# Kernel optimization log

Hardware: AMD Instinct MI355X
Metric: run time of the kernel (lower is better)

The kernel has to match this reference:

```python
import jax, jax.numpy as jnp
import numpy as np

E = 1280   # embed_dim
H = 16     # num_heads
D = E // H # head_dim = 80
S = 3072   # total tokens


def _rotate_half(x):
    x1, x2 = x[..., : D // 2], x[..., D // 2:]
    return jnp.concatenate((-x2, x1), axis=-1)


def setup_inputs() -> dict:
    key = jax.random.key(0)
    ks = jax.random.split(key, 7)
    x = jax.random.normal(ks[0], (S, E), dtype=jnp.float32)
    # rotary embeddings: cos/sin of random angles, shape (S, head_dim)
    ang = jax.random.uniform(ks[1], (S, D), dtype=jnp.float32) * (2 * np.pi)
    cos = jnp.cos(ang)
    sin = jnp.sin(ang)
    # 8 variable-length segments covering all S tokens
    cu_seqlens = jnp.array([0, 256, 640, 1024, 1536, 1920, 2304, 2688, 3072], dtype=jnp.int32)
    qkv_w = jax.random.normal(ks[2], (3 * E, E), dtype=jnp.float32) * 0.02
    qkv_b = jax.random.normal(ks[3], (3 * E,), dtype=jnp.float32) * 0.02
    proj_w = jax.random.normal(ks[4], (E, E), dtype=jnp.float32) * 0.02
    proj_b = jax.random.normal(ks[5], (E,), dtype=jnp.float32) * 0.02
    return {"x": x, "cu_seqlens": cu_seqlens, "cos": cos, "sin": sin,
            "qkv_w": qkv_w, "qkv_b": qkv_b, "proj_w": proj_w, "proj_b": proj_b}


def reference(x, cu_seqlens, cos, sin, qkv_w, qkv_b, proj_w, proj_b):
    # QKV projection: (S, 3E)
    qkv = x @ qkv_w.T + qkv_b
    q, k, v = jnp.split(qkv, 3, axis=-1)
    q = q.reshape(S, H, D)
    k = k.reshape(S, H, D)
    v = v.reshape(S, H, D)
    # inline RoPE, broadcast over heads (cos/sin: (S,1,D))
    c = cos[:, None, :]
    s = sin[:, None, :]
    q = q * c + _rotate_half(q) * s
    k = k * c + _rotate_half(k) * s
    # block-diagonal varlen attention: tokens attend only within their segment
    seg_ids = jnp.searchsorted(cu_seqlens, jnp.arange(S), side="right")  # (S,)
    mask = seg_ids[:, None] == seg_ids[None, :]                           # (S,S)
    scale = 1.0 / jnp.sqrt(jnp.asarray(D, dtype=q.dtype))
    scores = jnp.einsum("qhd,khd->hqk", q, k) * scale                    # (H,S,S)
    neg = jnp.finfo(scores.dtype).min
    scores = jnp.where(mask[None, :, :], scores, neg)
    attn = jax.nn.softmax(scores, axis=-1)
    out = jnp.einsum("hqk,khd->qhd", attn, v).reshape(S, E)
    return out @ proj_w.T + proj_b
```

## Files before the change

kernel.cpp:

```cpp
#include <hip/hip_runtime.h>
#include <hip/hip_bf16.h>

#define S_LEN 3072
#define E_DIM 1280
#define NH 16
#define HD 80
#define HDP 96
#define QKV_N 3840

typedef unsigned short u16;
typedef unsigned int u32;
typedef __bf16 bf16x8 __attribute__((ext_vector_type(8)));
typedef float f32x4 __attribute__((ext_vector_type(4)));

__device__ __forceinline__ u16 bf16_bits(float f) {
  __hip_bfloat16 b = __float2bfloat16(f);
  return *reinterpret_cast<u16*>(&b);
}
__device__ __forceinline__ float bf16_to_f(u16 u) {
  unsigned int x = ((unsigned int)u) << 16;
  return __uint_as_float(x);
}
__device__ __forceinline__ void gload_lds16(const u16* g, u16* l) {
  __builtin_amdgcn_global_load_lds(
      (const __attribute__((address_space(1))) void*)g,
      (__attribute__((address_space(3))) void*)l, 16, 0, 0);
}
__device__ __forceinline__ int imin(int a, int b) { return a < b ? a : b; }

#define XB_F4    983040
#define WQKV_F4  1228800
#define WPROJ_F4 409600
__global__ __launch_bounds__(256) void f32_to_bf16_3(const float* __restrict__ sx,
                                                     const float* __restrict__ sq,
                                                     const float* __restrict__ sp,
                                                     u16* __restrict__ dst) {
  int i = blockIdx.x * 256 + threadIdx.x;
  float4 v;
  if (i < XB_F4) v = reinterpret_cast<const float4*>(sx)[i];
  else if (i < XB_F4 + WQKV_F4) v = reinterpret_cast<const float4*>(sq)[i - XB_F4];
  else v = reinterpret_cast<const float4*>(sp)[i - XB_F4 - WQKV_F4];
  ushort4 o;
  o.x = bf16_bits(v.x); o.y = bf16_bits(v.y); o.z = bf16_bits(v.z); o.w = bf16_bits(v.w);
  reinterpret_cast<ushort4*>(dst)[i] = o;
}

template<int OUT_F32>
__global__ __launch_bounds__(256) void gemm_nt(const u16* __restrict__ A,
                                               const u16* __restrict__ B,
                                               const float* __restrict__ bias,
                                               void* __restrict__ Cout,
                                               int M, int N, int K, int nbx) {
  __shared__ u16 As[128 * 64];
  __shared__ u16 Bs[128 * 64];
  const int t = threadIdx.x;
  const int lane = t & 63;
  const int wave = t >> 6;
  const int l15 = lane & 15, l4 = lane >> 4;
  const int wm = (wave >> 1) * 64, wn = (wave & 1) * 64;

  const int nwg = gridDim.x;
  const int lg = (blockIdx.x & 7) * (nwg >> 3) + (blockIdx.x >> 3);
  const int m0 = (lg / nbx) * 128, n0 = (lg % nbx) * 128;

  const u16* gA[4];
  const u16* gB[4];
  u16* lA[4];
  u16* lB[4];
  #pragma unroll
  for (int i = 0; i < 4; ++i) {
    const int c = i * 256 + t;
    const int row = c >> 3;
    const int col = ((c & 7) ^ (row & 7)) * 8;
    gA[i] = A + (size_t)(m0 + row) * K + col;
    gB[i] = B + (size_t)(n0 + row) * K + col;
    lA[i] = &As[c * 8];
    lB[i] = &Bs[c * 8];
  }

  int aoff[4][2], boff[4][2];
  #pragma unroll
  for (int i = 0; i < 4; ++i)
    #pragma unroll
    for (int kk = 0; kk < 2; ++kk) {
      aoff[i][kk] = (wm + i * 16 + l15) * 64 + ((kk * 4 + l4) ^ (l15 & 7)) * 8;
      boff[i][kk] = (wn + i * 16 + l15) * 64 + ((kk * 4 + l4) ^ (l15 & 7)) * 8;
    }

  f32x4 acc[4][4] = {};

  const int nk = K >> 6;
  for (int kt = 0; kt < nk; ++kt) {
    const int k0 = kt << 6;
    #pragma unroll
    for (int i = 0; i < 4; ++i) gload_lds16(gA[i] + k0, lA[i]);
    #pragma unroll
    for (int i = 0; i < 4; ++i) gload_lds16(gB[i] + k0, lB[i]);
    __syncthreads();
    bf16x8 af[4][2], bfr[4][2];
    #pragma unroll
    for (int i = 0; i < 4; ++i)
      #pragma unroll
      for (int kk = 0; kk < 2; ++kk) {
        af[i][kk]  = *reinterpret_cast<const bf16x8*>(&As[aoff[i][kk]]);
        bfr[i][kk] = *reinterpret_cast<const bf16x8*>(&Bs[boff[i][kk]]);
      }
    __builtin_amdgcn_s_setprio(1);
    #pragma unroll
    for (int kk = 0; kk < 2; ++kk)
      #pragma unroll
      for (int i = 0; i < 4; ++i)
        #pragma unroll
        for (int j = 0; j < 4; ++j)
          acc[i][j] = __builtin_amdgcn_mfma_f32_16x16x32_bf16(af[i][kk], bfr[j][kk],
                                                              acc[i][j], 0, 0, 0);
    __builtin_amdgcn_s_setprio(0);
    __syncthreads();
  }

  #pragma unroll
  for (int i = 0; i < 4; ++i) {
    #pragma unroll
    for (int j = 0; j < 4; ++j) {
      const int col = n0 + wn + j * 16 + l15;
      const float bv = bias[col];
      const int rowb = m0 + wm + i * 16 + l4 * 4;
      #pragma unroll
      for (int r = 0; r < 4; ++r) {
        float v = acc[i][j][r] + bv;
        if (OUT_F32)
          reinterpret_cast<float*>(Cout)[(size_t)(rowb + r) * N + col] = v;
        else
          reinterpret_cast<u16*>(Cout)[(size_t)(rowb + r) * N + col] = bf16_bits(v);
      }
    }
  }
}

#define ROPE_NB 12288
#define VT_NB   1920
__global__ __launch_bounds__(256) void rope_vt(const u16* __restrict__ qkv,
                                               const float* __restrict__ cosb,
                                               const float* __restrict__ sinb,
                                               u16* __restrict__ qp,
                                               u16* __restrict__ kp,
                                               u16* __restrict__ vt) {
  const int b = blockIdx.x;
  const int t = threadIdx.x;
  if (b < ROPE_NB) {
    const int h = b / 768;
    const int sl = t >> 6;
    const int p = t & 63;
    const int s = (b % 768) * 4 + sl;
    const size_t ib = (size_t)s * QKV_N + h * HD;
    const size_t ob = ((size_t)h * S_LEN + s) * HDP;
    if (p < 40) {
      const float scale = 0.1118033988749895f;
      float q1 = bf16_to_f(qkv[ib + p]);
      float q2 = bf16_to_f(qkv[ib + 40 + p]);
      float k1 = bf16_to_f(qkv[ib + E_DIM + p]);
      float k2 = bf16_to_f(qkv[ib + E_DIM + 40 + p]);
      float c1 = cosb[(size_t)s * HD + p],      s1 = sinb[(size_t)s * HD + p];
      float c2 = cosb[(size_t)s * HD + 40 + p], s2 = sinb[(size_t)s * HD + 40 + p];
      qp[ob + p]      = bf16_bits((q1 * c1 - q2 * s1) * scale);
      qp[ob + 40 + p] = bf16_bits((q2 * c2 + q1 * s2) * scale);
      kp[ob + p]      = bf16_bits(k1 * c1 - k2 * s1);
      kp[ob + 40 + p] = bf16_bits(k2 * c2 + k1 * s2);
    } else if (p < 48) {
      const int pd = HD + (p - 40) * 2;
      qp[ob + pd] = 0; qp[ob + pd + 1] = 0;
      kp[ob + pd] = 0; kp[ob + pd + 1] = 0;
    }
  } else {
    const int idx = (b - ROPE_NB) * 256 + t;
    const int d = idx % HD;
    const int h = (idx / HD) % NH;
    const int sb = idx / (HD * NH);
    const int s0 = sb * 8;
    if (s0 >= S_LEN) return;
    u16 bb[8];
    #pragma unroll
    for (int j = 0; j < 8; ++j)
      bb[j] = qkv[(size_t)(s0 + j) * QKV_N + 2 * E_DIM + h * HD + d];
    uint4 pk;
    pk.x = bb[0] | ((unsigned)bb[1] << 16);
    pk.y = bb[2] | ((unsigned)bb[3] << 16);
    pk.z = bb[4] | ((unsigned)bb[5] << 16);
    pk.w = bb[6] | ((unsigned)bb[7] << 16);
    *reinterpret_cast<uint4*>(&vt[((size_t)h * HD + d) * S_LEN + s0]) = pk;
  }
}

__global__ __launch_bounds__(256, 3) void attn_fwd(const u16* __restrict__ qp,
                                                   const u16* __restrict__ kp,
                                                   const u16* __restrict__ vt,
                                                   const int* __restrict__ cu, int ncu,
                                                   u16* __restrict__ ao) {
  __shared__ u16 Ks[64 * 128];
  __shared__ u16 Vs[80 * 64];
  __shared__ u16 Pl[4][16][72];

  const int lg = ((blockIdx.x & 7) * 96) + (blockIdx.x >> 3);
  const int h = lg / 48;
  const int q0 = (lg % 48) * 64;

  const int t = threadIdx.x;
  const int wave = t >> 6;
  const int lane = t & 63;
  const int l15 = lane & 15, l4 = lane >> 4;
  const int qr = q0 + wave * 16;

  int lo = 0, hi = S_LEN;
  for (int i = 0; i + 1 < ncu; ++i) {
    int a = cu[i], b = cu[i + 1];
    if (q0 >= a && q0 < b) { lo = a; hi = b; }
  }
  const int nt = (hi - lo + 63) >> 6;

  const u16* qh = qp + (size_t)h * S_LEN * HDP;
  const u16* kh = kp + (size_t)h * S_LEN * HDP;
  const u16* vh = vt + (size_t)h * HD * S_LEN;

  bf16x8 qf[3];
  #pragma unroll
  for (int c = 0; c < 3; ++c)
    qf[c] = *reinterpret_cast<const bf16x8*>(&qh[(size_t)(qr + l15) * HDP + c * 32 + l4 * 8]);

  int kr[3], kcc[3], kw[3];
  #pragma unroll
  for (int i = 0; i < 3; ++i) {
    const int c2 = i * 256 + t;
    kr[i] = c2 / 12; kcc[i] = c2 % 12;
    kw[i] = kr[i] * 128 + ((kcc[i] ^ (kr[i] & 7)) * 8);
  }
  int vd[3], vcc[3], vwo[3];
  #pragma unroll
  for (int i = 0; i < 3; ++i) {
    const int c2 = i * 256 + t;
    vd[i] = c2 >> 3; vcc[i] = c2 & 7;
    vwo[i] = vd[i] * 64 + ((vcc[i] ^ (vd[i] & 7)) * 8);
  }
  const bool v2 = (t < 128);

  {
    const int kbv = imin(lo, S_LEN - 64);
    bf16x8 kstg[3], vstg[3];
    #pragma unroll
    for (int i = 0; i < 3; ++i)
      kstg[i] = *reinterpret_cast<const bf16x8*>(
          &kh[(size_t)imin(lo + kr[i], S_LEN - 1) * HDP + kcc[i] * 8]);
    #pragma unroll
    for (int i = 0; i < 2; ++i)
      vstg[i] = *reinterpret_cast<const bf16x8*>(&vh[(size_t)vd[i] * S_LEN + kbv + vcc[i] * 8]);
    if (v2)
      vstg[2] = *reinterpret_cast<const bf16x8*>(&vh[(size_t)vd[2] * S_LEN + kbv + vcc[2] * 8]);
    #pragma unroll
    for (int i = 0; i < 3; ++i) *reinterpret_cast<bf16x8*>(&Ks[kw[i]]) = kstg[i];
    #pragma unroll
    for (int i = 0; i < 2; ++i) *reinterpret_cast<bf16x8*>(&Vs[vwo[i]]) = vstg[i];
    if (v2) *reinterpret_cast<bf16x8*>(&Vs[vwo[2]]) = vstg[2];
    __syncthreads();
  }

  f32x4 oacc[5] = {};
  float mrow = -INFINITY, lrow = 0.f;
  const float L2E = 1.4426950408889634f;

  int pwr[4];
  #pragma unroll
  for (int f = 0; f < 4; ++f)
    pwr[f] = ((f * 2 + (l4 >> 1)) ^ (l15 & 7)) * 8 + (l4 & 1) * 4;
  int prd[2];
  #pragma unroll
  for (int kc = 0; kc < 2; ++kc)
    prd[kc] = ((kc * 4 + l4) ^ (l15 & 7)) * 8;

  for (int ti = 0; ti < nt; ++ti) {
    const int kb = lo + ti * 64;
    const bool more = (ti + 1) < nt;

    bf16x8 kstg[3], vstg[3];
    if (more) {
      const int kb2 = kb + 64;
      const int kbv = imin(kb2, S_LEN - 64);
      #pragma unroll
      for (int i = 0; i < 3; ++i)
        kstg[i] = *reinterpret_cast<const bf16x8*>(
            &kh[(size_t)imin(kb2 + kr[i], S_LEN - 1) * HDP + kcc[i] * 8]);
      #pragma unroll
      for (int i = 0; i < 2; ++i)
        vstg[i] = *reinterpret_cast<const bf16x8*>(&vh[(size_t)vd[i] * S_LEN + kbv + vcc[i] * 8]);
      if (v2)
        vstg[2] = *reinterpret_cast<const bf16x8*>(&vh[(size_t)vd[2] * S_LEN + kbv + vcc[2] * 8]);
    }

    f32x4 sc[4];
    #pragma unroll
    for (int f = 0; f < 4; ++f) { f32x4 z = {0.f, 0.f, 0.f, 0.f}; sc[f] = z; }
    __builtin_amdgcn_s_setprio(1);
    #pragma unroll
    for (int f = 0; f < 4; ++f)
      #pragma unroll
      for (int c = 0; c < 3; ++c) {
        bf16x8 kf = *reinterpret_cast<const bf16x8*>(
            &Ks[(f * 16 + l15) * 128 + (((c * 4 + l4) ^ (l15 & 7)) * 8)]);
        sc[f] = __builtin_amdgcn_mfma_f32_16x16x32_bf16(kf, qf[c], sc[f], 0, 0, 0);
      }
    __builtin_amdgcn_s_setprio(0);

    if (kb + 64 > hi) {
      #pragma unroll
      for (int f = 0; f < 4; ++f)
        #pragma unroll
        for (int r = 0; r < 4; ++r)
          if (kb + f * 16 + l4 * 4 + r >= hi) sc[f][r] = -INFINITY;
    }

    float tm = -INFINITY;
    #pragma unroll
    for (int f = 0; f < 4; ++f)
      #pragma unroll
      for (int r = 0; r < 4; ++r) tm = fmaxf(tm, sc[f][r]);
    tm = fmaxf(tm, __shfl_xor(tm, 16, 64));
    tm = fmaxf(tm, __shfl_xor(tm, 32, 64));

    if (__any(tm > mrow + 8.f)) {
      float mn = fmaxf(mrow, tm);
      float corr = exp2f((mrow - mn) * L2E);
      mrow = mn;
      lrow *= corr;
      #pragma unroll
      for (int df = 0; df < 5; ++df)
        #pragma unroll
        for (int r = 0; r < 4; ++r) oacc[df][r] *= corr;
    }

    float rs = 0.f;
    #pragma unroll
    for (int f = 0; f < 4; ++f) {
      float p0 = exp2f((sc[f][0] - mrow) * L2E);
      float p1 = exp2f((sc[f][1] - mrow) * L2E);
      float p2 = exp2f((sc[f][2] - mrow) * L2E);
      float p3 = exp2f((sc[f][3] - mrow) * L2E);
      rs += (p0 + p1) + (p2 + p3);
      uint2 w;
      w.x = (u32)bf16_bits(p0) | ((u32)bf16_bits(p1) << 16);
      w.y = (u32)bf16_bits(p2) | ((u32)bf16_bits(p3) << 16);
      *reinterpret_cast<uint2*>(&Pl[wave][l15][pwr[f]]) = w;
    }
    rs += __shfl_xor(rs, 16, 64);
    rs += __shfl_xor(rs, 32, 64);
    lrow += rs;

    asm volatile("s_waitcnt lgkmcnt(0)" ::: "memory");

    __builtin_amdgcn_s_setprio(1);
    #pragma unroll
    for (int kc = 0; kc < 2; ++kc) {
      bf16x8 pf = *reinterpret_cast<const bf16x8*>(&Pl[wave][l15][prd[kc]]);
      #pragma unroll
      for (int df = 0; df < 5; ++df) {
        bf16x8 vf = *reinterpret_cast<const bf16x8*>(
            &Vs[(df * 16 + l15) * 64 + (((kc * 4 + l4) ^ (l15 & 7)) * 8)]);
        oacc[df] = __builtin_amdgcn_mfma_f32_16x16x32_bf16(vf, pf, oacc[df], 0, 0, 0);
      }
    }
    __builtin_amdgcn_s_setprio(0);

    if (more) {
      __syncthreads();
      #pragma unroll
      for (int i = 0; i < 3; ++i) *reinterpret_cast<bf16x8*>(&Ks[kw[i]]) = kstg[i];
      #pragma unroll
      for (int i = 0; i < 2; ++i) *reinterpret_cast<bf16x8*>(&Vs[vwo[i]]) = vstg[i];
      if (v2) *reinterpret_cast<bf16x8*>(&Vs[vwo[2]]) = vstg[2];
      __syncthreads();
    }
  }

  const float inv = 1.0f / lrow;
  #pragma unroll
  for (int df = 0; df < 5; ++df) {
    ushort4 o;
    o.x = bf16_bits(oacc[df][0] * inv);
    o.y = bf16_bits(oacc[df][1] * inv);
    o.z = bf16_bits(oacc[df][2] * inv);
    o.w = bf16_bits(oacc[df][3] * inv);
    *reinterpret_cast<ushort4*>(
        &ao[(size_t)(qr + l15) * E_DIM + h * HD + df * 16 + l4 * 4]) = o;
  }
}

extern "C" void kernel_launch(void* const* d_in, const int* in_sizes, int n_in,
                              void* d_out, int out_size, void* d_ws, size_t ws_size,
                              hipStream_t stream) {
  const float* x      = (const float*)d_in[0];
  const int*   cu     = (const int*)d_in[1];
  const float* cosb   = (const float*)d_in[2];
  const float* sinb   = (const float*)d_in[3];
  const float* qkv_w  = (const float*)d_in[4];
  const float* qkv_b  = (const float*)d_in[5];
  const float* proj_w = (const float*)d_in[6];
  const float* proj_b = (const float*)d_in[7];
  float* out = (float*)d_out;

  u16* xb     = (u16*)d_ws;
  u16* wqkvb  = xb     + (size_t)S_LEN * E_DIM;
  u16* wprojb = wqkvb  + (size_t)3 * E_DIM * E_DIM;
  u16* qkv    = wprojb + (size_t)E_DIM * E_DIM;
  u16* qp     = qkv    + (size_t)S_LEN * QKV_N;
  u16* kp     = qp     + (size_t)NH * S_LEN * HDP;
  u16* vt     = kp     + (size_t)NH * S_LEN * HDP;
  u16* attn   = vt     + (size_t)NH * HD * S_LEN;

  const int nf4 = XB_F4 + WQKV_F4 + WPROJ_F4;
  f32_to_bf16_3<<<nf4 / 256, 256, 0, stream>>>(x, qkv_w, proj_w, xb);

  gemm_nt<0><<<(QKV_N / 128) * (S_LEN / 128), 256, 0, stream>>>(
      xb, wqkvb, qkv_b, qkv, S_LEN, QKV_N, E_DIM, QKV_N / 128);

  rope_vt<<<ROPE_NB + VT_NB, 256, 0, stream>>>(qkv, cosb, sinb, qp, kp, vt);

  attn_fwd<<<NH * (S_LEN / 64), 256, 0, stream>>>(qp, kp, vt, cu, in_sizes[1], attn);

  gemm_nt<1><<<(E_DIM / 128) * (S_LEN / 128), 256, 0, stream>>>(
      attn, wprojb, proj_b, out, S_LEN, E_DIM, E_DIM, E_DIM / 128);
}
```

Before: 109.8 us.

## Fuse RoPE and V transpose into QKV GEMM epilogue via interleaved weight rows

Permutes the Q/K rows of the QKV weight and bias during the conversion pass so that rotate-half partner columns land in adjacent lanes. The QKV GEMM epilogue then applies RoPE with a lane shuffle and writes padded Q/K and transposed V directly. This removes the intermediate bf16 QKV buffer and the separate rope_vt kernel along with their global memory round trip. In exchange the epilogue issues scattered 2-byte stores and per-element cos/sin loads, and zeroing of the pad columns moves into the prep kernel.

After: 121.7 us. 10.9% more time.

```diff
diff --git a/kernel.cpp b/kernel.cpp
--- a/kernel.cpp
+++ b/kernel.cpp
@@ -28,28 +28,175 @@
 }
 __device__ __forceinline__ int imin(int a, int b) { return a < b ? a : b; }
 
+__device__ __forceinline__ int qk_orig(int c) {
+  if (c >= 2 * E_DIM) return c;
+  int h = c / 80, c80 = c % 80;
+  int p = c80 >> 1;
+  return h * 80 + ((c80 & 1) ? 40 + p : p);
+}
+
 #define XB_F4    983040
 #define WQKV_F4  1228800
 #define WPROJ_F4 409600
-__global__ __launch_bounds__(256) void f32_to_bf16_3(const float* __restrict__ sx,
-                                                     const float* __restrict__ sq,
-                                                     const float* __restrict__ sp,
-                                                     u16* __restrict__ dst) {
-  int i = blockIdx.x * 256 + threadIdx.x;
-  float4 v;
-  if (i < XB_F4) v = reinterpret_cast<const float4*>(sx)[i];
-  else if (i < XB_F4 + WQKV_F4) v = reinterpret_cast<const float4*>(sq)[i - XB_F4];
-  else v = reinterpret_cast<const float4*>(sp)[i - XB_F4 - WQKV_F4];
-  ushort4 o;
-  o.x = bf16_bits(v.x); o.y = bf16_bits(v.y); o.z = bf16_bits(v.z); o.w = bf16_bits(v.w);
-  reinterpret_cast<ushort4*>(dst)[i] = o;
-}
-
-template<int OUT_F32>
+#define CV_BLKS  10240
+#define PB_BLKS  15
+#define PAD_BLKS 768
+__global__ __launch_bounds__(256) void prep(const float* __restrict__ sx,
+                                            const float* __restrict__ sq,
+                                            const float* __restrict__ sp,
+                                            const float* __restrict__ qb,
+                                            u16* __restrict__ dst,
+                                            float* __restrict__ pb,
+                                            u16* __restrict__ qp,
+                                            u16* __restrict__ kp) {
+  const int b = blockIdx.x, t = threadIdx.x;
+  if (b < CV_BLKS) {
+    int i = b * 256 + t;
+    float4 v;
+    if (i < XB_F4) v = reinterpret_cast<const float4*>(sx)[i];
+    else if (i < XB_F4 + WQKV_F4) {
+      int j = i - XB_F4;
+      int row = j / 320, c4 = j % 320;
+      v = reinterpret_cast<const float4*>(sq)[(size_t)qk_orig(row) * 320 + c4];
+    } else v = reinterpret_cast<const float4*>(sp)[i - XB_F4 - WQKV_F4];
+    ushort4 o;
+    o.x = bf16_bits(v.x); o.y = bf16_bits(v.y); o.z = bf16_bits(v.z); o.w = bf16_bits(v.w);
+    reinterpret_cast<ushort4*>(dst)[i] = o;
+  } else if (b < CV_BLKS + PB_BLKS) {
+    int i = (b - CV_BLKS) * 256 + t;
+    if (i < QKV_N) pb[i] = qb[qk_orig(i)];
+  } else {
+    int u = (b - CV_BLKS - PB_BLKS) * 256 + t;
+    const int per = NH * S_LEN * 2;
+    u16* d = (u < per) ? qp : kp;
+    int r2 = (u < per) ? u : u - per;
+    int hs = r2 >> 1, half = r2 & 1;
+    uint4 z = {0u, 0u, 0u, 0u};
+    *reinterpret_cast<uint4*>(&d[(size_t)hs * HDP + 80 + half * 8]) = z;
+  }
+}
+
+__global__ __launch_bounds__(256) void gemm_qkv(const u16* __restrict__ A,
+                                                const u16* __restrict__ B,
+                                                const float* __restrict__ pb,
+                                                const float* __restrict__ cosb,
+                                                const float* __restrict__ sinb,
+                                                u16* __restrict__ qp,
+                                                u16* __restrict__ kp,
+                                                u16* __restrict__ vt) {
+  __shared__ u16 As[128 * 64];
+  __shared__ u16 Bs[128 * 64];
+  const int K = E_DIM;
+  const int t = threadIdx.x;
+  const int lane = t & 63;
+  const int wave = t >> 6;
+  const int l15 = lane & 15, l4 = lane >> 4;
+  const int wm = (wave >> 1) * 64, wn = (wave & 1) * 64;
+
+  const int nwg = gridDim.x;
+  const int lg = (blockIdx.x & 7) * (nwg >> 3) + (blockIdx.x >> 3);
+  const int m0 = (lg / 30) * 128, n0 = (lg % 30) * 128;
+
+  const u16* gA[4];
+  const u16* gB[4];
+  u16* lA[4];
+  u16* lB[4];
+  #pragma unroll
+  for (int i = 0; i < 4; ++i) {
+    const int c = i * 256 + t;
+    const int row = c >> 3;
+    const int col = ((c & 7) ^ (row & 7)) * 8;
+    gA[i] = A + (size_t)(m0 + row) * K + col;
+    gB[i] = B + (size_t)(n0 + row) * K + col;
+    lA[i] = &As[c * 8];
+    lB[i] = &Bs[c * 8];
+  }
+
+  int aoff[4][2], boff[4][2];
+  #pragma unroll
+  for (int i = 0; i < 4; ++i)
+    #pragma unroll
+    for (int kk = 0; kk < 2; ++kk) {
+      aoff[i][kk] = (wm + i * 16 + l15) * 64 + ((kk * 4 + l4) ^ (l15 & 7)) * 8;
+      boff[i][kk] = (wn + i * 16 + l15) * 64 + ((kk * 4 + l4) ^ (l15 & 7)) * 8;
+    }
+
+  f32x4 acc[4][4] = {};
+
+  const int nk = K >> 6;
+  for (int kt = 0; kt < nk; ++kt) {
+    const int k0 = kt << 6;
+    #pragma unroll
+    for (int i = 0; i < 4; ++i) gload_lds16(gA[i] + k0, lA[i]);
+    #pragma unroll
+    for (int i = 0; i < 4; ++i) gload_lds16(gB[i] + k0, lB[i]);
+    __syncthreads();
+    bf16x8 af[4][2], bfr[4][2];
+    #pragma unroll
+    for (int i = 0; i < 4; ++i)
+      #pragma unroll
+      for (int kk = 0; kk < 2; ++kk) {
+        af[i][kk]  = *reinterpret_cast<const bf16x8*>(&As[aoff[i][kk]]);
+        bfr[i][kk] = *reinterpret_cast<const bf16x8*>(&Bs[boff[i][kk]]);
+      }
+    __builtin_amdgcn_s_setprio(1);
+    #pragma unroll
+    for (int kk = 0; kk < 2; ++kk)
+      #pragma unroll
+      for (int i = 0; i < 4; ++i)
+        #pragma unroll
+        for (int j = 0; j < 4; ++j)
+          acc[i][j] = __builtin_amdgcn_mfma_f32_16x16x32_bf16(af[i][kk], bfr[j][kk],
+                                                              acc[i][j], 0, 0, 0);
+    __builtin_amdgcn_s_setprio(0);
+    __syncthreads();
+  }
+
+  const bool isqk = (n0 < 2 * E_DIM);
+  const bool isq  = (n0 < E_DIM);
+  const float scaleq = 0.1118033988749895f;
+  #pragma unroll
+  for (int i = 0; i < 4; ++i) {
+    const int srow = m0 + wm + i * 16 + l4 * 4;
+    #pragma unroll
+    for (int j = 0; j < 4; ++j) {
+      const int col = n0 + wn + j * 16 + l15;
+      const float bv = pb[col];
+      float vv[4];
+      #pragma unroll
+      for (int r = 0; r < 4; ++r) vv[r] = acc[i][j][r] + bv;
+      if (isqk) {
+        const int c80 = col % 80;
+        const int hh = col / 80;
+        const int parity = c80 & 1;
+        const int peff = (c80 >> 1) + (parity ? 40 : 0);
+        u16* dst = isq ? qp : kp;
+        const int hb = isq ? hh : hh - NH;
+        const float sc = isq ? scaleq : 1.0f;
+        #pragma unroll
+        for (int r = 0; r < 4; ++r) {
+          float pv = __shfl_xor(vv[r], 1, 64);
+          float cs = cosb[(size_t)(srow + r) * HD + peff];
+          float sn = sinb[(size_t)(srow + r) * HD + peff];
+          float o = parity ? fmaf(pv, sn, vv[r] * cs) : fmaf(-pv, sn, vv[r] * cs);
+          dst[((size_t)hb * S_LEN + srow + r) * HDP + c80] = bf16_bits(o * sc);
+        }
+      } else {
+        const int cv = col - 2 * E_DIM;
+        const int hb = cv / 80, d = cv % 80;
+        ushort4 o;
+        o.x = bf16_bits(vv[0]); o.y = bf16_bits(vv[1]);
+        o.z = bf16_bits(vv[2]); o.w = bf16_bits(vv[3]);
+        *reinterpret_cast<ushort4*>(&vt[((size_t)hb * HD + d) * S_LEN + srow]) = o;
+      }
+    }
+  }
+}
+
 __global__ __launch_bounds__(256) void gemm_nt(const u16* __restrict__ A,
                                                const u16* __restrict__ B,
                                                const float* __restrict__ bias,
-                                               void* __restrict__ Cout,
+                                               float* __restrict__ Cout,
                                                int M, int N, int K, int nbx) {
   __shared__ u16 As[128 * 64];
   __shared__ u16 Bs[128 * 64];
@@ -126,68 +273,9 @@
       const float bv = bias[col];
       const int rowb = m0 + wm + i * 16 + l4 * 4;
       #pragma unroll
-      for (int r = 0; r < 4; ++r) {
-        float v = acc[i][j][r] + bv;
-        if (OUT_F32)
-          reinterpret_cast<float*>(Cout)[(size_t)(rowb + r) * N + col] = v;
-        else
-          reinterpret_cast<u16*>(Cout)[(size_t)(rowb + r) * N + col] = bf16_bits(v);
-      }
-    }
-  }
-}
-
-#define ROPE_NB 12288
-#define VT_NB   1920
-__global__ __launch_bounds__(256) void rope_vt(const u16* __restrict__ qkv,
-                                               const float* __restrict__ cosb,
-                                               const float* __restrict__ sinb,
-                                               u16* __restrict__ qp,
-                                               u16* __restrict__ kp,
-                                               u16* __restrict__ vt) {
-  const int b = blockIdx.x;
-  const int t = threadIdx.x;
-  if (b < ROPE_NB) {
-    const int h = b / 768;
-    const int sl = t >> 6;
-    const int p = t & 63;
-    const int s = (b % 768) * 4 + sl;
-    const size_t ib = (size_t)s * QKV_N + h * HD;
-    const size_t ob = ((size_t)h * S_LEN + s) * HDP;
-    if (p < 40) {
-      const float scale = 0.1118033988749895f;
-      float q1 = bf16_to_f(qkv[ib + p]);
-      float q2 = bf16_to_f(qkv[ib + 40 + p]);
-      float k1 = bf16_to_f(qkv[ib + E_DIM + p]);
-      float k2 = bf16_to_f(qkv[ib + E_DIM + 40 + p]);
-      float c1 = cosb[(size_t)s * HD + p],      s1 = sinb[(size_t)s * HD + p];
-      float c2 = cosb[(size_t)s * HD + 40 + p], s2 = sinb[(size_t)s * HD + 40 + p];
-      qp[ob + p]      = bf16_bits((q1 * c1 - q2 * s1) * scale);
-      qp[ob + 40 + p] = bf16_bits((q2 * c2 + q1 * s2) * scale);
-      kp[ob + p]      = bf16_bits(k1 * c1 - k2 * s1);
-      kp[ob + 40 + p] = bf16_bits(k2 * c2 + k1 * s2);
-    } else if (p < 48) {
-      const int pd = HD + (p - 40) * 2;
-      qp[ob + pd] = 0; qp[ob + pd + 1] = 0;
-      kp[ob + pd] = 0; kp[ob + pd + 1] = 0;
-    }
-  } else {
-    const int idx = (b - ROPE_NB) * 256 + t;
-    const int d = idx % HD;
-    const int h = (idx / HD) % NH;
-    const int sb = idx / (HD * NH);
-    const int s0 = sb * 8;
-    if (s0 >= S_LEN) return;
-    u16 bb[8];
-    #pragma unroll
-    for (int j = 0; j < 8; ++j)
-      bb[j] = qkv[(size_t)(s0 + j) * QKV_N + 2 * E_DIM + h * HD + d];
-    uint4 pk;
-    pk.x = bb[0] | ((unsigned)bb[1] << 16);
-    pk.y = bb[2] | ((unsigned)bb[3] << 16);
-    pk.z = bb[4] | ((unsigned)bb[5] << 16);
-    pk.w = bb[6] | ((unsigned)bb[7] << 16);
-    *reinterpret_cast<uint4*>(&vt[((size_t)h * HD + d) * S_LEN + s0]) = pk;
+      for (int r = 0; r < 4; ++r)
+        Cout[(size_t)(rowb + r) * N + col] = acc[i][j][r] + bv;
+    }
   }
 }
 
@@ -407,22 +495,20 @@
   u16* xb     = (u16*)d_ws;
   u16* wqkvb  = xb     + (size_t)S_LEN * E_DIM;
   u16* wprojb = wqkvb  + (size_t)3 * E_DIM * E_DIM;
-  u16* qkv    = wprojb + (size_t)E_DIM * E_DIM;
-  u16* qp     = qkv    + (size_t)S_LEN * QKV_N;
+  u16* qp     = wprojb + (size_t)E_DIM * E_DIM;
   u16* kp     = qp     + (size_t)NH * S_LEN * HDP;
   u16* vt     = kp     + (size_t)NH * S_LEN * HDP;
   u16* attn   = vt     + (size_t)NH * HD * S_LEN;
-
-  const int nf4 = XB_F4 + WQKV_F4 + WPROJ_F4;
-  f32_to_bf16_3<<<nf4 / 256, 256, 0, stream>>>(x, qkv_w, proj_w, xb);
-
-  gemm_nt<0><<<(QKV_N / 128) * (S_LEN / 128), 256, 0, stream>>>(
-      xb, wqkvb, qkv_b, qkv, S_LEN, QKV_N, E_DIM, QKV_N / 128);
-
-  rope_vt<<<ROPE_NB + VT_NB, 256, 0, stream>>>(qkv, cosb, sinb, qp, kp, vt);
+  float* pb   = (float*)(attn + (size_t)S_LEN * E_DIM);
+
+  prep<<<CV_BLKS + PB_BLKS + PAD_BLKS, 256, 0, stream>>>(
+      x, qkv_w, proj_w, qkv_b, xb, pb, qp, kp);
+
+  gemm_qkv<<<(QKV_N / 128) * (S_LEN / 128), 256, 0, stream>>>(
+      xb, wqkvb, pb, cosb, sinb, qp, kp, vt);
 
   attn_fwd<<<NH * (S_LEN / 64), 256, 0, stream>>>(qp, kp, vt, cu, in_sizes[1], attn);
 
-  gemm_nt<1><<<(E_DIM / 128) * (S_LEN / 128), 256, 0, stream>>>(
+  gemm_nt<<<(E_DIM / 128) * (S_LEN / 128), 256, 0, stream>>>(
       attn, wprojb, proj_b, out, S_LEN, E_DIM, E_DIM, E_DIM / 128);
 }
```
